# Performance work log

Hardware: AMD Instinct MI355X
Metric: run time of the kernel (lower is better)

## Reference

```python
import jax, jax.numpy as jnp
import numpy as np

N_NODES = 100000
N_EDGES = 3200000
HID = 128
NUM_ATTR = 10000
K = 3
EPS = 1e-5


def setup_inputs() -> dict:
    key = jax.random.key(0)
    ks = jax.random.split(key, 8)
    x_idx = jax.random.randint(ks[0], (N_NODES,), 0, NUM_ATTR)
    edge_index = jax.random.randint(ks[1], (2, N_EDGES), 0, N_NODES)
    edge_weight = jax.random.uniform(ks[2], (N_EDGES,), dtype=jnp.float32)
    emb = jax.random.normal(ks[3], (NUM_ATTR, HID), dtype=jnp.float32) * 0.1
    Wt = jax.random.normal(ks[4], (K, HID, HID), dtype=jnp.float32) * (1.0 / np.sqrt(HID))
    bt = jnp.zeros((K, HID), jnp.float32)
    Wc = jax.random.normal(ks[5], (K, 2 * HID, HID), dtype=jnp.float32) * (1.0 / np.sqrt(2 * HID))
    bc = jnp.zeros((K, HID), jnp.float32)
    cg_gamma = jnp.ones((K, HID), jnp.float32)
    cg_beta = jnp.zeros((K, HID), jnp.float32)
    cg_alpha = jnp.ones((K, HID), jnp.float32)
    gn_gamma = jnp.ones((K - 1, HID), jnp.float32)
    gn_beta = jnp.zeros((K - 1, HID), jnp.float32)
    gn_alpha = jnp.ones((K - 1, HID), jnp.float32)
    return dict(x_idx=x_idx, edge_index=edge_index, edge_weight=edge_weight, emb=emb,
                Wt=Wt, bt=bt, Wc=Wc, bc=bc, cg_gamma=cg_gamma, cg_beta=cg_beta,
                cg_alpha=cg_alpha, gn_gamma=gn_gamma, gn_beta=gn_beta, gn_alpha=gn_alpha)


def graph_norm(x, gamma, beta, alpha):
    # GraphNorm over node dim: out = gamma*(x - alpha*mean)/sqrt(var+eps) + beta
    mean = jnp.mean(x, axis=0, keepdims=True)
    sub = x - alpha * mean
    var = jnp.mean(sub * sub, axis=0, keepdims=True)
    return gamma * sub * jax.lax.rsqrt(var + EPS) + beta


def build_mean_adj_weights(edge_index, edge_weight, n_nodes):
    # aggr='mean': w_e = edge_weight_e / deg[row_e], deg from row sums (deg<0.5 -> +1)
    row = edge_index[0]
    deg = jax.ops.segment_sum(edge_weight, row, num_segments=n_nodes)
    deg = jnp.where(deg < 0.5, deg + 1.0, deg)
    inv_deg = 1.0 / deg
    return edge_weight * inv_deg[row]


def conv_layer(x_, row, col, w, Wt, bt, Wc, bc, g, b, a):
    h = jax.nn.relu(x_ @ Wt + bt)                                   # [N, HID]
    m = jax.ops.segment_sum(w[:, None] * h[col], row, num_segments=x_.shape[0])  # adj @ h
    m = graph_norm(m, g, b, a)
    return jnp.concatenate([m, x_], axis=-1) @ Wc + bc


def reference(x_idx, edge_index, edge_weight, emb, Wt, bt, Wc, bc,
              cg_gamma, cg_beta, cg_alpha, gn_gamma, gn_beta, gn_alpha):
    row, col = edge_index[0], edge_index[1]
    w = build_mean_adj_weights(edge_index, edge_weight, x_idx.shape[0])
    x = emb[x_idx]  # embedding lookup; dropout p=0 -> identity
    for i in range(K - 1):
        x = conv_layer(x, row, col, w, Wt[i], bt[i], Wc[i], bc[i],
                       cg_gamma[i], cg_beta[i], cg_alpha[i])
        x = graph_norm(x, gn_gamma[i], gn_beta[i], gn_alpha[i])
        x = jax.nn.relu(x)
    x = conv_layer(x, row, col, w, Wt[K - 1], bt[K - 1], Wc[K - 1], bc[K - 1],
                   cg_gamma[K - 1], cg_beta[K - 1], cg_alpha[K - 1])
    return x
```

## Files before the change

kernel.cpp:

```cpp
#include <hip/hip_runtime.h>
#include <cstdio>


#define HID 128

typedef __attribute__((ext_vector_type(8))) short short8;
typedef __attribute__((ext_vector_type(4))) float floatx4;
typedef __attribute__((ext_vector_type(8))) _Float16 half8;
typedef __attribute__((ext_vector_type(2))) _Float16 half2v;

__device__ __forceinline__ unsigned short f2bf(float f) {
    unsigned u = __float_as_uint(f);
    unsigned r = (u + 0x7FFFu + ((u >> 16) & 1u)) >> 16;
    return (unsigned short)r;
}
__device__ __forceinline__ float bflo(unsigned u) { return __uint_as_float(u << 16); }
__device__ __forceinline__ float bfhi(unsigned u) { return __uint_as_float(u & 0xFFFF0000u); }

#define NB 512
#define RPB 196
#define CAPB 8192
#define TILE_A 2048

__global__ __launch_bounds__(256) void k_binA(
    const int* __restrict__ row, const int* __restrict__ col,
    const float* __restrict__ ew, int2* __restrict__ binned,
    unsigned* __restrict__ cursor, int E) {
    __shared__ int2 stag[TILE_A];
    __shared__ unsigned short bof[TILE_A];
    __shared__ unsigned hist[NB], scanned[NB], bump[NB];
    __shared__ int delta[NB];
    __shared__ unsigned scanw[256];
    int t = threadIdx.x;
    int tileBase = blockIdx.x * TILE_A;
    int tcnt = min(TILE_A, E - tileBase);

    hist[t] = 0; hist[t + 256] = 0;
    __syncthreads();

    int myb[8]; int2 myv[8];
#pragma unroll
    for (int i = 0; i < 8; ++i) {
        int idx = t + i * 256;
        if (idx < tcnt) {
            int e = tileBase + idx;
            int r = row[e];
            int c = col[e];
            float w = ew[e];
            int b = r / RPB;
            int rl = r - b * RPB;
            myb[i] = b;
            myv[i] = make_int2((rl << 17) | c, __float_as_int(w));
            atomicAdd(&hist[b], 1u);
        } else {
            myb[i] = -1;
            myv[i] = make_int2(0, 0);
        }
    }
    __syncthreads();

    unsigned h0 = hist[2 * t], h1 = hist[2 * t + 1];
    unsigned p = h0 + h1;
    scanw[t] = p;
    __syncthreads();
    for (int o = 1; o < 256; o <<= 1) {
        unsigned x = (t >= o) ? scanw[t - o] : 0u;
        __syncthreads();
        scanw[t] += x;
        __syncthreads();
    }
    unsigned excl = scanw[t] - p;
    scanned[2 * t] = excl;          bump[2 * t] = excl;
    scanned[2 * t + 1] = excl + h0; bump[2 * t + 1] = excl + h0;
    __syncthreads();

#pragma unroll
    for (int j = 0; j < 2; ++j) {
        int b = t + j * 256;
        unsigned c = hist[b];
        if (c) {
            unsigned old = atomicAdd(&cursor[b], c);
            delta[b] = (int)((unsigned)b * CAPB + old) - (int)scanned[b];
        }
    }
    __syncthreads();

#pragma unroll
    for (int i = 0; i < 8; ++i) {
        if (myb[i] >= 0) {
            unsigned s = atomicAdd(&bump[myb[i]], 1u);
            stag[s] = myv[i];
            bof[s] = (unsigned short)myb[i];
        }
    }
    __syncthreads();

    for (int i = t; i < tcnt; i += 256) {
        int b = bof[i];
        int dst = delta[b] + i;
        if (dst < (b + 1) * CAPB) binned[dst] = stag[i];
    }
}

__global__ void k_bscan(const unsigned* __restrict__ cursor, unsigned* __restrict__ outbase) {
    __shared__ unsigned scanw[256];
    int t = threadIdx.x;
    unsigned h0 = min(cursor[2 * t], (unsigned)CAPB);
    unsigned h1 = min(cursor[2 * t + 1], (unsigned)CAPB);
    unsigned p = h0 + h1;
    scanw[t] = p;
    __syncthreads();
    for (int o = 1; o < 256; o <<= 1) {
        unsigned x = (t >= o) ? scanw[t - o] : 0u;
        __syncthreads();
        scanw[t] += x;
        __syncthreads();
    }
    unsigned excl = scanw[t] - p;
    outbase[2 * t] = excl;
    outbase[2 * t + 1] = excl + h0;
}

__global__ __launch_bounds__(256) void k_binB(
    const int2* __restrict__ binned, const unsigned* __restrict__ cursor,
    const unsigned* __restrict__ outbase, int2* __restrict__ edge_s,
    unsigned* __restrict__ endp, unsigned* __restrict__ cntg, int N) {
    __shared__ unsigned hist[256], bump[256], scanw[256];
    __shared__ float wsum[256], inv[256];
    int b = blockIdx.x, t = threadIdx.x;
    size_t base_in = (size_t)b * CAPB;
    unsigned cntb = min(cursor[b], (unsigned)CAPB);
    unsigned outb = outbase[b];

    hist[t] = 0;
    wsum[t] = 0.f;
    __syncthreads();
    for (unsigned i = t; i < cntb; i += 256) {
        int2 v = binned[base_in + i];
        unsigned rl = ((unsigned)v.x) >> 17;
        atomicAdd(&hist[rl], 1u);
        atomicAdd(&wsum[rl], __int_as_float(v.y));
    }
    __syncthreads();

    unsigned h = hist[t];
    scanw[t] = h;
    __syncthreads();
    for (int o = 1; o < 256; o <<= 1) {
        unsigned x = (t >= o) ? scanw[t - o] : 0u;
        __syncthreads();
        scanw[t] += x;
        __syncthreads();
    }
    unsigned excl = scanw[t] - h;
    bump[t] = excl;
    float d = wsum[t];
    d = (d < 0.5f) ? d + 1.0f : d;
    inv[t] = 1.0f / d;
    int grow = b * RPB + t;
    if (t < RPB && grow < N) {
        endp[grow] = outb + excl + h;
        cntg[grow] = h;
    }
    __syncthreads();

    for (unsigned i = t; i < cntb; i += 256) {
        int2 v = binned[base_in + i];
        unsigned rl = ((unsigned)v.x) >> 17;
        unsigned pos = outb + atomicAdd(&bump[rl], 1u);
        float w = __int_as_float(v.y) * inv[rl];
        edge_s[pos] = make_int2(v.x & 0x1FFFF, __float_as_int(w));
    }
}

__global__ void k_prepw(const float* __restrict__ Wt, const float* __restrict__ Wc,
                        unsigned short* __restrict__ WtT, unsigned short* __restrict__ WcT) {
    int tid = blockIdx.x * blockDim.x + threadIdx.x;
    const int T1 = 3 * 128 * 128;
    const int T2 = 3 * 256 * 128;
    if (tid < T1) {
        int l = tid >> 14, rem = tid & 16383;
        int n = rem >> 7, k = rem & 127;
        WtT[tid] = f2bf(Wt[l * 16384 + k * 128 + n]);
    } else if (tid < T1 + T2) {
        int t2 = tid - T1;
        int l = t2 >> 15, rem = t2 & 32767;
        int n = rem >> 8, k = rem & 255;
        WcT[t2] = f2bf(Wc[l * 32768 + k * 128 + n]);
    }
}

#define GM_ROWS 128
#define LDSP 136

__global__ __launch_bounds__(256) void k_gemm(
    const float* __restrict__ X1, const int* __restrict__ G1,
    const float* __restrict__ AB1, int relu1, int xf1,
    const float* __restrict__ X2, const int* __restrict__ G2,
    const float* __restrict__ AB2, int relu2, int xf2,
    const unsigned short* __restrict__ Wn, int Kpitch, int nstage,
    const float* __restrict__ bias, void* __restrict__ Y,
    int relu_out, int out_mode, float* __restrict__ Sout, int N) {
    __shared__ unsigned short Ws[128 * LDSP];
    __shared__ unsigned short Xs[128 * LDSP];
    __shared__ float sred[4][256];
    int t = threadIdx.x;
    int rowBase = blockIdx.x * GM_ROWS;
    int lane = t & 63, wave = t >> 6;
    int quad = lane >> 4, l16 = lane & 15;

    floatx4 acc[2][8];
#pragma unroll
    for (int i = 0; i < 2; ++i)
#pragma unroll
        for (int j = 0; j < 8; ++j) acc[i][j] = (floatx4){0.f, 0.f, 0.f, 0.f};

    int kg = (t & 15) * 8;
    int r0 = t >> 4;

    for (int s = 0; s < nstage; ++s) {
        const float* Xp = s ? X2 : X1;
        const int* Gp = s ? G2 : G1;
        const float* ABp = s ? AB2 : AB1;
        int rl = s ? relu2 : relu1;
        int xf = s ? xf2 : xf1;
        int koff = s * 128;

#pragma unroll
        for (int j = 0; j < 8; ++j) {
            int n = r0 + 16 * j;
            *(short8*)&Ws[n * LDSP + kg] =
                *(const short8*)&Wn[(size_t)n * Kpitch + koff + kg];
        }
        floatx4 Av0 = {1.f, 1.f, 1.f, 1.f}, Av1 = Av0;
        floatx4 Bv0 = {0.f, 0.f, 0.f, 0.f}, Bv1 = Bv0;
        if (ABp) {
            Av0 = *(const floatx4*)&ABp[kg];
            Av1 = *(const floatx4*)&ABp[kg + 4];
            Bv0 = *(const floatx4*)&ABp[HID + kg];
            Bv1 = *(const floatx4*)&ABp[HID + kg + 4];
        }
#pragma unroll
        for (int j = 0; j < 8; ++j) {
            int r = r0 + 16 * j;
            int grow = rowBase + r;
            floatx4 x0 = {0.f, 0.f, 0.f, 0.f}, x1 = x0;
            if (grow < N) {
                size_t srow = Gp ? (size_t)Gp[grow] : (size_t)grow;
                if (xf) {
                    half8 mv = *(const half8*)&((const _Float16*)Xp)[srow * HID + kg];
#pragma unroll
                    for (int c = 0; c < 4; ++c) {
                        x0[c] = (float)mv[c];
                        x1[c] = (float)mv[c + 4];
                    }
                } else {
                    x0 = *(const floatx4*)&Xp[srow * HID + kg];
                    x1 = *(const floatx4*)&Xp[srow * HID + kg + 4];
                }
            }
            if (ABp) {
#pragma unroll
                for (int c = 0; c < 4; ++c) {
                    x0[c] = fmaf(x0[c], Av0[c], Bv0[c]);
                    x1[c] = fmaf(x1[c], Av1[c], Bv1[c]);
                }
                if (rl) {
#pragma unroll
                    for (int c = 0; c < 4; ++c) {
                        x0[c] = fmaxf(x0[c], 0.f);
                        x1[c] = fmaxf(x1[c], 0.f);
                    }
                }
            }
            short8 st;
            st[0] = (short)f2bf(x0[0]); st[1] = (short)f2bf(x0[1]);
            st[2] = (short)f2bf(x0[2]); st[3] = (short)f2bf(x0[3]);
            st[4] = (short)f2bf(x1[0]); st[5] = (short)f2bf(x1[1]);
            st[6] = (short)f2bf(x1[2]); st[7] = (short)f2bf(x1[3]);
            *(short8*)&Xs[r * LDSP + kg] = st;
        }
        __syncthreads();

#pragma unroll
        for (int ks = 0; ks < 4; ++ks) {
            int kb = ks * 32 + quad * 8;
            short8 a0 = *(const short8*)&Xs[(wave * 32 + l16) * LDSP + kb];
            short8 a1 = *(const short8*)&Xs[(wave * 32 + 16 + l16) * LDSP + kb];
#pragma unroll
            for (int ni = 0; ni < 8; ++ni) {
                short8 b = *(const short8*)&Ws[(ni * 16 + l16) * LDSP + kb];
                acc[0][ni] = __builtin_amdgcn_mfma_f32_16x16x32_bf16(a0, b, acc[0][ni], 0, 0, 0);
                acc[1][ni] = __builtin_amdgcn_mfma_f32_16x16x32_bf16(a1, b, acc[1][ni], 0, 0, 0);
            }
        }
        __syncthreads();
    }

    float s1[8], s2[8];
#pragma unroll
    for (int ni = 0; ni < 8; ++ni) { s1[ni] = 0.f; s2[ni] = 0.f; }

#pragma unroll
    for (int mi = 0; mi < 2; ++mi) {
#pragma unroll
        for (int ni = 0; ni < 8; ++ni) {
            int gcol = ni * 16 + l16;
            float bv = bias[gcol];
#pragma unroll
            for (int reg = 0; reg < 4; ++reg) {
                int grow = rowBase + wave * 32 + mi * 16 + quad * 4 + reg;
                if (grow < N) {
                    float v = acc[mi][ni][reg] + bv;
                    if (relu_out) v = fmaxf(v, 0.f);
                    s1[ni] += v;
                    s2[ni] += v * v;
                    if (out_mode == 1)
                        ((unsigned short*)Y)[(size_t)grow * HID + gcol] = f2bf(v);
                    else if (out_mode == 2)
                        ((_Float16*)Y)[(size_t)grow * HID + gcol] = (_Float16)v;
                    else
                        ((float*)Y)[(size_t)grow * HID + gcol] = v;
                }
            }
        }
    }

    if (Sout) {
#pragma unroll
        for (int ni = 0; ni < 8; ++ni) {
            s1[ni] += __shfl_xor(s1[ni], 16);
            s1[ni] += __shfl_xor(s1[ni], 32);
            s2[ni] += __shfl_xor(s2[ni], 16);
            s2[ni] += __shfl_xor(s2[ni], 32);
        }
        if (lane < 16) {
#pragma unroll
            for (int ni = 0; ni < 8; ++ni) {
                sred[wave][ni * 16 + l16] = s1[ni];
                sred[wave][128 + ni * 16 + l16] = s2[ni];
            }
        }
        __syncthreads();
        float v = sred[0][t & 255];
        if (t < 256) {
            v = sred[0][t] + sred[1][t] + sred[2][t] + sred[3][t];
            atomicAdd(&Sout[(blockIdx.x & 15) * 256 + t], v);
        }
    }
}

#define AGG_R 4

__global__ __launch_bounds__(256) void k_agg(
    const unsigned short* __restrict__ H, const int2* __restrict__ es,
    const unsigned* __restrict__ endp, const unsigned* __restrict__ cnt,
    _Float16* __restrict__ Mh, float* __restrict__ Spart, int N) {
    __shared__ float sb[4][256];
    int t = threadIdx.x;
    int wv = t >> 6, lane = t & 63;
    int grp = lane >> 4;
    int l16 = lane & 15;
    const uint4* __restrict__ H4 = (const uint4*)H;
    int rowBase = blockIdx.x * (4 * AGG_R) + wv * AGG_R;
    int fo = l16 * 8 + grp * 2;
    float s1a = 0.f, s1b = 0.f, s2a = 0.f, s2b = 0.f;

    for (int j = 0; j < AGG_R; ++j) {
        int rowi = rowBase + j;
        if (rowi >= N) break;
        unsigned e = endp[rowi];
        unsigned p = e - cnt[rowi];

        float acc[8];
#pragma unroll
        for (int i = 0; i < 8; ++i) acc[i] = 0.f;

        for (; p + 15 < e; p += 16) {
            int2 ee[4];
#pragma unroll
            for (int q = 0; q < 4; ++q) ee[q] = es[p + 4 * q + grp];
            uint4 hh[4];
#pragma unroll
            for (int q = 0; q < 4; ++q)
                hh[q] = H4[(size_t)ee[q].x * 16 + l16];
            __builtin_amdgcn_sched_barrier(0);
#pragma unroll
            for (int q = 0; q < 4; ++q) {
                float w = __int_as_float(ee[q].y);
                acc[0] = fmaf(w, bflo(hh[q].x), acc[0]);
                acc[1] = fmaf(w, bfhi(hh[q].x), acc[1]);
                acc[2] = fmaf(w, bflo(hh[q].y), acc[2]);
                acc[3] = fmaf(w, bfhi(hh[q].y), acc[3]);
                acc[4] = fmaf(w, bflo(hh[q].z), acc[4]);
                acc[5] = fmaf(w, bfhi(hh[q].z), acc[5]);
                acc[6] = fmaf(w, bflo(hh[q].w), acc[6]);
                acc[7] = fmaf(w, bfhi(hh[q].w), acc[7]);
            }
        }
        for (; p < e; p += 4) {
            unsigned idx = p + grp;
            int2 e0 = make_int2(0, 0);
            if (idx < e) e0 = es[idx];
            uint4 h = H4[(size_t)e0.x * 16 + l16];
            float w = __int_as_float(e0.y);
            acc[0] = fmaf(w, bflo(h.x), acc[0]);
            acc[1] = fmaf(w, bfhi(h.x), acc[1]);
            acc[2] = fmaf(w, bflo(h.y), acc[2]);
            acc[3] = fmaf(w, bfhi(h.y), acc[3]);
            acc[4] = fmaf(w, bflo(h.z), acc[4]);
            acc[5] = fmaf(w, bfhi(h.z), acc[5]);
            acc[6] = fmaf(w, bflo(h.w), acc[6]);
            acc[7] = fmaf(w, bfhi(h.w), acc[7]);
        }

#pragma unroll
        for (int i = 0; i < 8; ++i) {
            acc[i] += __shfl_xor(acc[i], 16);
            acc[i] += __shfl_xor(acc[i], 32);
        }
        float va = (grp & 2) ? ((grp & 1) ? acc[6] : acc[4])
                             : ((grp & 1) ? acc[2] : acc[0]);
        float vb = (grp & 2) ? ((grp & 1) ? acc[7] : acc[5])
                             : ((grp & 1) ? acc[3] : acc[1]);
        half2v st;
        st[0] = (_Float16)va;
        st[1] = (_Float16)vb;
        *(half2v*)&Mh[(size_t)rowi * HID + fo] = st;
        s1a += va; s1b += vb;
        s2a += va * va; s2b += vb * vb;
    }

    sb[wv][fo] = s1a;
    sb[wv][fo + 1] = s1b;
    sb[wv][128 + fo] = s2a;
    sb[wv][128 + fo + 1] = s2b;
    __syncthreads();
    {
        float v = sb[0][t] + sb[1][t] + sb[2][t] + sb[3][t];
        atomicAdd(&Spart[(blockIdx.x & 15) * 256 + t], v);
    }
}

__global__ void k_finalize(const float* __restrict__ S, const float* __restrict__ gamma,
                           const float* __restrict__ beta, const float* __restrict__ alpha,
                           float* __restrict__ AB, float invN) {
    int f = threadIdx.x;
    float sum = 0.f, sq = 0.f;
#pragma unroll
    for (int c = 0; c < 16; ++c) {
        sum += S[c * 256 + f];
        sq += S[c * 256 + 128 + f];
    }
    float mu = sum * invN;
    float ex2 = sq * invN;
    float a = alpha[f];
    float var = ex2 - 2.f * a * mu * mu + a * a * mu * mu;
    float rs = rsqrtf(var + 1e-5f);
    float A = gamma[f] * rs;
    float B = beta[f] - A * a * mu;
    AB[f] = A;
    AB[HID + f] = B;
}

extern "C" void kernel_launch(void* const* d_in, const int* in_sizes, int n_in,
                              void* d_out, int out_size, void* d_ws, size_t ws_size,
                              hipStream_t stream) {
    const int*   x_idx = (const int*)d_in[0];
    const int*   ei    = (const int*)d_in[1];
    const float* ew    = (const float*)d_in[2];
    const float* emb   = (const float*)d_in[3];
    const float* Wt    = (const float*)d_in[4];
    const float* bt    = (const float*)d_in[5];
    const float* Wc    = (const float*)d_in[6];
    const float* bc    = (const float*)d_in[7];
    const float* cg_g  = (const float*)d_in[8];
    const float* cg_b  = (const float*)d_in[9];
    const float* cg_a  = (const float*)d_in[10];
    const float* gn_g  = (const float*)d_in[11];
    const float* gn_b  = (const float*)d_in[12];
    const float* gn_a  = (const float*)d_in[13];
    const int N = in_sizes[0];
    const int E = in_sizes[2];
    const int* row = ei;
    const int* col = ei + E;

    char* ws = (char*)d_ws;
    size_t off = 0;
    auto alloc = [&](size_t bytes) -> void* {
        size_t o = (off + 511) & ~(size_t)511;
        off = o + bytes;
        return (void*)(ws + o);
    };
    const int SSTRIDE = 16 * 256;
    unsigned* cursor = (unsigned*)alloc(NB * 4);
    float*    Spart  = (float*)alloc(5 * SSTRIDE * 4);
    size_t zero_end = off;
    unsigned* outbase = (unsigned*)alloc(NB * 4);
    unsigned* endp    = (unsigned*)alloc((size_t)N * 4);
    unsigned* cnt     = (unsigned*)alloc((size_t)N * 4);
    float*    AB      = (float*)alloc(5 * 256 * 4);
    unsigned short* WtT = (unsigned short*)alloc((size_t)3 * 128 * 128 * 2);
    unsigned short* WcT = (unsigned short*)alloc((size_t)3 * 128 * 256 * 2);
    int2*     binned  = (int2*)alloc((size_t)NB * CAPB * 8);
    int2*     edge_s  = (int2*)alloc((size_t)E * 8);
    unsigned short* H = (unsigned short*)alloc((size_t)N * HID * 2);
    _Float16* Xh      = (_Float16*)alloc((size_t)N * HID * 2);
    _Float16* Mh      = (_Float16*)alloc((size_t)N * HID * 2);
    if (off > ws_size) {
        fprintf(stderr, "kernel_launch: ws too small (%zu > %zu)\n", off, ws_size);
        return;
    }

    hipMemsetAsync(d_ws, 0, zero_end, stream);

    k_prepw<<<(3 * 128 * 128 + 3 * 256 * 128 + 255) / 256, 256, 0, stream>>>(Wt, Wc, WtT, WcT);
    k_binA<<<(E + TILE_A - 1) / TILE_A, 256, 0, stream>>>(row, col, ew, binned, cursor, E);
    k_bscan<<<1, 256, 0, stream>>>(cursor, outbase);
    k_binB<<<NB, 256, 0, stream>>>(binned, cursor, outbase, edge_s, endp, cnt, N);

    int gemm_blocks = (N + GM_ROWS - 1) / GM_ROWS;
    auto gemm = [&](const float* X1, const int* G1, const float* AB1, int rl1, int xf1,
                    const float* X2, const int* G2, const float* AB2, int rl2, int xf2,
                    const unsigned short* Wn, int Kpitch, int nstage,
                    const float* bias, void* Y, int relu_out, int out_mode,
                    float* Sout) {
        k_gemm<<<gemm_blocks, 256, 0, stream>>>(X1, G1, AB1, rl1, xf1,
                                                X2, G2, AB2, rl2, xf2,
                                                Wn, Kpitch, nstage, bias, Y,
                                                relu_out, out_mode, Sout, N);
    };
    int aggB = (N + 4 * AGG_R - 1) / (4 * AGG_R);
    auto agg = [&](int stage) {
        k_agg<<<aggB, 256, 0, stream>>>(H, edge_s, endp, cnt, Mh,
                                        Spart + stage * SSTRIDE, N);
    };
    auto fin = [&](int stage, const float* g, const float* b, const float* a) {
        k_finalize<<<1, 128, 0, stream>>>(Spart + stage * SSTRIDE, g, b, a,
                                          AB + stage * 256, 1.0f / (float)N);
    };

    gemm(emb, x_idx, nullptr, 0, 0,
         nullptr, nullptr, nullptr, 0, 0,
         WtT, 128, 1, bt, H, 1, 1, nullptr);
    agg(0);
    fin(0, cg_g, cg_b, cg_a);
    gemm((const float*)Mh, nullptr, AB + 0 * 256, 0, 1,
         emb, x_idx, nullptr, 0, 0,
         WcT, 256, 2, bc, Xh, 0, 2, Spart + 1 * SSTRIDE);
    fin(1, gn_g, gn_b, gn_a);

    gemm((const float*)Xh, nullptr, AB + 1 * 256, 1, 1,
         nullptr, nullptr, nullptr, 0, 0,
         WtT + 16384, 128, 1, bt + 128, H, 1, 1, nullptr);
    agg(2);
    fin(2, cg_g + 128, cg_b + 128, cg_a + 128);
    gemm((const float*)Mh, nullptr, AB + 2 * 256, 0, 1,
         (const float*)Xh, nullptr, AB + 1 * 256, 1, 1,
         WcT + 32768, 256, 2, bc + 128, Xh, 0, 2, Spart + 3 * SSTRIDE);
    fin(3, gn_g + 128, gn_b + 128, gn_a + 128);

    gemm((const float*)Xh, nullptr, AB + 3 * 256, 1, 1,
         nullptr, nullptr, nullptr, 0, 0,
         WtT + 2 * 16384, 128, 1, bt + 256, H, 1, 1, nullptr);
    agg(4);
    fin(4, cg_g + 256, cg_b + 256, cg_a + 256);
    gemm((const float*)Mh, nullptr, AB + 4 * 256, 0, 1,
         (const float*)Xh, nullptr, AB + 3 * 256, 1, 1,
         WcT + 2 * 32768, 256, 2, bc + 256, d_out, 0, 0, nullptr);
}
```

Measured before the change: 785.2 us.

## Use hardware bf16 pack conversion, batch GEMM loads, keep layer output in fp32

Replaces the software round-to-nearest bf16 conversion with the v_cvt_pk_bf16_f32 instruction, both when staging tiles into LDS and when writing the H output. The global loads in the GEMM staging loop are now all issued before the conversions, so more loads are in flight at once. The intermediate layer output X changes from fp16 to fp32, which doubles its read and write traffic but drops the fp16 rounding step. The larger buffer also raises workspace usage.

```diff
diff --git a/kernel.cpp b/kernel.cpp
--- a/kernel.cpp
+++ b/kernel.cpp
@@ -16,6 +16,15 @@
 }
 __device__ __forceinline__ float bflo(unsigned u) { return __uint_as_float(u << 16); }
 __device__ __forceinline__ float bfhi(unsigned u) { return __uint_as_float(u & 0xFFFF0000u); }
+
+__device__ __forceinline__ unsigned cvt_pk_bf16(float lo, float hi) {
+    unsigned r;
+    asm("v_cvt_pk_bf16_f32 %0, %1, %2" : "=v"(r) : "v"(lo), "v"(hi));
+    return r;
+}
+__device__ __forceinline__ unsigned short f2bf_hw(float v) {
+    return (unsigned short)(cvt_pk_bf16(v, v) & 0xFFFFu);
+}
 
 #define NB 512
 #define RPB 196
@@ -240,25 +249,31 @@
             Bv0 = *(const floatx4*)&ABp[HID + kg];
             Bv1 = *(const floatx4*)&ABp[HID + kg + 4];
         }
+        floatx4 xa[8], xb[8];
 #pragma unroll
         for (int j = 0; j < 8; ++j) {
-            int r = r0 + 16 * j;
-            int grow = rowBase + r;
-            floatx4 x0 = {0.f, 0.f, 0.f, 0.f}, x1 = x0;
+            int grow = rowBase + r0 + 16 * j;
+            xa[j] = (floatx4){0.f, 0.f, 0.f, 0.f};
+            xb[j] = xa[j];
             if (grow < N) {
                 size_t srow = Gp ? (size_t)Gp[grow] : (size_t)grow;
                 if (xf) {
                     half8 mv = *(const half8*)&((const _Float16*)Xp)[srow * HID + kg];
 #pragma unroll
                     for (int c = 0; c < 4; ++c) {
-                        x0[c] = (float)mv[c];
-                        x1[c] = (float)mv[c + 4];
+                        xa[j][c] = (float)mv[c];
+                        xb[j][c] = (float)mv[c + 4];
                     }
                 } else {
-                    x0 = *(const floatx4*)&Xp[srow * HID + kg];
-                    x1 = *(const floatx4*)&Xp[srow * HID + kg + 4];
+                    xa[j] = *(const floatx4*)&Xp[srow * HID + kg];
+                    xb[j] = *(const floatx4*)&Xp[srow * HID + kg + 4];
                 }
             }
+        }
+#pragma unroll
+        for (int j = 0; j < 8; ++j) {
+            int r = r0 + 16 * j;
+            floatx4 x0 = xa[j], x1 = xb[j];
             if (ABp) {
 #pragma unroll
                 for (int c = 0; c < 4; ++c) {
@@ -273,12 +288,12 @@
                     }
                 }
             }
-            short8 st;
-            st[0] = (short)f2bf(x0[0]); st[1] = (short)f2bf(x0[1]);
-            st[2] = (short)f2bf(x0[2]); st[3] = (short)f2bf(x0[3]);
-            st[4] = (short)f2bf(x1[0]); st[5] = (short)f2bf(x1[1]);
-            st[6] = (short)f2bf(x1[2]); st[7] = (short)f2bf(x1[3]);
-            *(short8*)&Xs[r * LDSP + kg] = st;
+            uint4 st;
+            st.x = cvt_pk_bf16(x0[0], x0[1]);
+            st.y = cvt_pk_bf16(x0[2], x0[3]);
+            st.z = cvt_pk_bf16(x1[0], x1[1]);
+            st.w = cvt_pk_bf16(x1[2], x1[3]);
+            *(uint4*)&Xs[r * LDSP + kg] = st;
         }
         __syncthreads();
 
@@ -316,7 +331,7 @@
                     s1[ni] += v;
                     s2[ni] += v * v;
                     if (out_mode == 1)
-                        ((unsigned short*)Y)[(size_t)grow * HID + gcol] = f2bf(v);
+                        ((unsigned short*)Y)[(size_t)grow * HID + gcol] = f2bf_hw(v);
                     else if (out_mode == 2)
                         ((_Float16*)Y)[(size_t)grow * HID + gcol] = (_Float16)v;
                     else
@@ -505,7 +520,7 @@
     int2*     binned  = (int2*)alloc((size_t)NB * CAPB * 8);
     int2*     edge_s  = (int2*)alloc((size_t)E * 8);
     unsigned short* H = (unsigned short*)alloc((size_t)N * HID * 2);
-    _Float16* Xh      = (_Float16*)alloc((size_t)N * HID * 2);
+    float*    X       = (float*)alloc((size_t)N * HID * 4);
     _Float16* Mh      = (_Float16*)alloc((size_t)N * HID * 2);
     if (off > ws_size) {
         fprintf(stderr, "kernel_launch: ws too small (%zu > %zu)\n", off, ws_size);
@@ -547,25 +562,25 @@
     fin(0, cg_g, cg_b, cg_a);
     gemm((const float*)Mh, nullptr, AB + 0 * 256, 0, 1,
          emb, x_idx, nullptr, 0, 0,
-         WcT, 256, 2, bc, Xh, 0, 2, Spart + 1 * SSTRIDE);
+         WcT, 256, 2, bc, X, 0, 0, Spart + 1 * SSTRIDE);
     fin(1, gn_g, gn_b, gn_a);
 
-    gemm((const float*)Xh, nullptr, AB + 1 * 256, 1, 1,
+    gemm(X, nullptr, AB + 1 * 256, 1, 0,
          nullptr, nullptr, nullptr, 0, 0,
          WtT + 16384, 128, 1, bt + 128, H, 1, 1, nullptr);
     agg(2);
     fin(2, cg_g + 128, cg_b + 128, cg_a + 128);
     gemm((const float*)Mh, nullptr, AB + 2 * 256, 0, 1,
-         (const float*)Xh, nullptr, AB + 1 * 256, 1, 1,
-         WcT + 32768, 256, 2, bc + 128, Xh, 0, 2, Spart + 3 * SSTRIDE);
+         X, nullptr, AB + 1 * 256, 1, 0,
+         WcT + 32768, 256, 2, bc + 128, X, 0, 0, Spart + 3 * SSTRIDE);
     fin(3, gn_g + 128, gn_b + 128, gn_a + 128);
 
-    gemm((const float*)Xh, nullptr, AB + 3 * 256, 1, 1,
+    gemm(X, nullptr, AB + 3 * 256, 1, 0,
          nullptr, nullptr, nullptr, 0, 0,
          WtT + 2 * 16384, 128, 1, bt + 256, H, 1, 1, nullptr);
     agg(4);
     fin(4, cg_g + 256, cg_b + 256, cg_a + 256);
     gemm((const float*)Mh, nullptr, AB + 4 * 256, 0, 1,
-         (const float*)Xh, nullptr, AB + 3 * 256, 1, 1,
+         X, nullptr, AB + 3 * 256, 1, 0,
          WcT + 2 * 32768, 256, 2, bc + 256, d_out, 0, 0, nullptr);
 }
```

Result: no change. 783.5 us (-0.2%).
